# Kernel tuning notes

Measured on AMD Instinct MI355X. Metric: run time of the kernel, lower is better.

## Reference

```python
import jax, jax.numpy as jnp
import numpy as np

B, S, D, A = 16, 2048, 512, 512

def setup_inputs() -> dict:
    key = jax.random.key(0)
    ks = jax.random.split(key, 7)
    scale = 1.0 / np.sqrt(D)
    return {
        "query": jax.random.normal(ks[0], (B, S, D), dtype=jnp.float32),
        "key_": jax.random.normal(ks[1], (B, S, D), dtype=jnp.float32),
        "value": jax.random.normal(ks[2], (B, S, D), dtype=jnp.float32),
        "Wq": jax.random.normal(ks[3], (D, A), dtype=jnp.float32) * scale,
        "Wk": jax.random.normal(ks[4], (D, A), dtype=jnp.float32) * scale,
        "Wv": jax.random.normal(ks[5], (D, A), dtype=jnp.float32) * scale,
        "Ws": jax.random.normal(ks[6], (A, 1), dtype=jnp.float32) * (1.0 / np.sqrt(A)),
    }

def reference(query, key_, value, Wq, Wk, Wv, Ws):
    # Dense projections (no bias): [B,S,D] @ [D,A] -> [B,S,A]
    q = jnp.einsum("bsd,da->bsa", query, Wq)
    k = jnp.einsum("bsd,da->bsa", key_, Wk)
    v = jnp.einsum("bsd,da->bsa", value, Wv)
    # Additive (Bahdanau) scores: tanh(q+k) @ Ws -> [B,S]
    scores = jnp.einsum("bsa,a->bs", jnp.tanh(q + k), Ws[:, 0])
    attention_weights = jax.nn.softmax(scores, axis=1)[..., None]  # [B,S,1]
    context_vector = jnp.sum(attention_weights * v, axis=1)        # [B,A]
    return context_vector, attention_weights
```

## Files before the change

### kernel.cpp

```cpp
#include <hip/hip_runtime.h>
#include <hip/hip_bf16.h>
#include <stdint.h>

#define B_ 16
#define S_ 2048
#define D_ 512
#define A_ 512

typedef __attribute__((ext_vector_type(4))) float f32x4;
typedef __attribute__((ext_vector_type(8))) short bf16x8;

__device__ inline unsigned short f2bf(float f) {
  union { float f; unsigned int u; } c; c.f = f;
  unsigned int u = c.u;
  unsigned int r = (u + 0x7fffu + ((u >> 16) & 1u)) >> 16;
  return (unsigned short)r;
}

__device__ inline unsigned pk2bf(float x, float y) {
  __hip_bfloat162 p = __float22bfloat162_rn(float2{x, y});
  union { __hip_bfloat162 h; unsigned u; } c; c.h = p;
  return c.u;
}

__device__ inline float fast_tanh(float x) {
  float e = __expf(2.0f * x);
  return 1.0f - 2.0f * __builtin_amdgcn_rcpf(e + 1.0f);
}

__device__ inline void gload_lds16(const void* g, void* l) {
  __builtin_amdgcn_global_load_lds((const __attribute__((address_space(1))) void*)g,
                                   (__attribute__((address_space(3))) void*)l, 16, 0, 0);
}

__global__ __launch_bounds__(256) void k0_pack_w(const float* __restrict__ Wq,
                                                 const float* __restrict__ Wk,
                                                 unsigned short* __restrict__ WT) {
  __shared__ unsigned short tile[64][65];
  int bid = blockIdx.x;
  int dt = bid & 15, at = bid >> 4;
  int d0 = dt * 64, a0 = at * 64;
  int t = threadIdx.x;
  int col = t & 63, rbase = t >> 6;
#pragma unroll
  for (int r8 = 0; r8 < 16; ++r8) {
    int row = r8 * 4 + rbase;
    int dcat = d0 + row;
    float f = (dcat < 512) ? Wq[(size_t)dcat * 512 + a0 + col]
                           : Wk[(size_t)(dcat - 512) * 512 + a0 + col];
    tile[row][col] = f2bf(f);
  }
  __syncthreads();
#pragma unroll
  for (int r8 = 0; r8 < 16; ++r8) {
    int arow = r8 * 4 + rbase;
    WT[(size_t)(a0 + arow) * 1024 + d0 + col] = tile[col][arow];
  }
}

__global__ __launch_bounds__(512, 2) void k1_scores(
    const float* __restrict__ Q, const float* __restrict__ K,
    const unsigned short* __restrict__ WT, const float* __restrict__ Wsv,
    float* __restrict__ score) {
  __shared__ unsigned short Al[2][128 * 32];
  __shared__ unsigned short Bl[2][512 * 32];

  const int t = threadIdx.x;
  const int lane = t & 63, w = t >> 6;
  const int frow = lane & 15, fsl = lane >> 4;
  const int row0 = (int)blockIdx.x * 128;

  const int ar = t >> 2, ak = (t & 3) * 8;
  const int abyte = ar * 64 + (((t & 3) ^ ((ar >> 1) & 3)) * 16);

  float4 rA0[2], rA1[2];

  auto issueA = [&](int p, float4* r) {
    const float* src = (p < 16) ? Q : K;
    const float* ap = src + (size_t)(row0 + ar) * 512 + ((p * 32) & 511) + ak;
    r[0] = *(const float4*)(ap);
    r[1] = *(const float4*)(ap + 4);
  };
  auto writeA = [&](const float4* r, int buf) {
    uint4 d;
    d.x = pk2bf(r[0].x, r[0].y);
    d.y = pk2bf(r[0].z, r[0].w);
    d.z = pk2bf(r[1].x, r[1].y);
    d.w = pk2bf(r[1].z, r[1].w);
    *(uint4*)((char*)&Al[buf][0] + abyte) = d;
  };
  auto stageB = [&](int p, int buf) {
#pragma unroll
    for (int q = 0; q < 4; ++q) {
      int pc = (w * 4 + q) * 64 + lane;
      int row = pc >> 2;
      int sl = (pc & 3) ^ ((row >> 1) & 3);
      const char* g = (const char*)WT + (size_t)row * 2048 + p * 64 + sl * 16;
      gload_lds16(g, (char*)&Bl[buf][0] + (size_t)(w * 4 + q) * 1024);
    }
  };

  f32x4 acc[8][4];
#pragma unroll
  for (int m = 0; m < 8; ++m)
#pragma unroll
    for (int n = 0; n < 4; ++n) acc[m][n] = (f32x4){0.f, 0.f, 0.f, 0.f};

  const int ch = (fsl ^ ((frow >> 1) & 3)) * 16;

  auto doMfma = [&](int CUR) {
    bf16x8 af[8], bfr[4];
#pragma unroll
    for (int m = 0; m < 8; ++m)
      af[m] = *(const bf16x8*)((const char*)&Al[CUR][0] + (m * 16 + frow) * 64 + ch);
#pragma unroll
    for (int n = 0; n < 4; ++n)
      bfr[n] = *(const bf16x8*)((const char*)&Bl[CUR][0] + (w * 64 + n * 16 + frow) * 64 + ch);
    __builtin_amdgcn_s_setprio(1);
#pragma unroll
    for (int m = 0; m < 8; ++m)
#pragma unroll
      for (int n = 0; n < 4; ++n)
        acc[m][n] = __builtin_amdgcn_mfma_f32_16x16x32_bf16(af[m], bfr[n], acc[m][n], 0, 0, 0);
    __builtin_amdgcn_s_setprio(0);
  };

  issueA(0, rA0);
  stageB(0, 0);
  __builtin_amdgcn_sched_barrier(0);
  issueA(1, rA1);
  writeA(rA0, 0);
  asm volatile("s_waitcnt vmcnt(2) lgkmcnt(0)" ::: "memory");
  __builtin_amdgcn_s_barrier();

  auto phase = [&](int p, int CUR, float4* rCur, const float4* rNext) {
    stageB(p + 1, CUR ^ 1);
    __builtin_amdgcn_sched_barrier(0);
    issueA(p + 2, rCur);
    doMfma(CUR);
    writeA(rNext, CUR ^ 1);
    asm volatile("s_waitcnt vmcnt(2) lgkmcnt(0)" ::: "memory");
    __builtin_amdgcn_s_barrier();
  };

  for (int kt2 = 0; kt2 < 15; ++kt2) {
    phase(2 * kt2 + 0, 0, rA0, rA1);
    phase(2 * kt2 + 1, 1, rA1, rA0);
  }

  stageB(31, 1);
  doMfma(0);
  writeA(rA1, 1);
  asm volatile("s_waitcnt vmcnt(0) lgkmcnt(0)" ::: "memory");
  __builtin_amdgcn_s_barrier();
  doMfma(1);

  float wsv[4];
#pragma unroll
  for (int n = 0; n < 4; ++n) wsv[n] = Wsv[w * 64 + n * 16 + frow];
  __syncthreads();
  float* scw = (float*)&Al[0][0];
#pragma unroll
  for (int m = 0; m < 8; ++m) {
#pragma unroll
    for (int ii = 0; ii < 4; ++ii) {
      float s = 0.f;
#pragma unroll
      for (int n = 0; n < 4; ++n)
        s += fast_tanh(acc[m][n][ii]) * wsv[n];
      s += __shfl_xor(s, 1);
      s += __shfl_xor(s, 2);
      s += __shfl_xor(s, 4);
      s += __shfl_xor(s, 8);
      if (frow == 0) scw[w * 128 + m * 16 + fsl * 4 + ii] = s;
    }
  }
  __syncthreads();
  if (t < 128) {
    float s = 0.f;
#pragma unroll
    for (int ww = 0; ww < 8; ++ww) s += scw[ww * 128 + t];
    score[row0 + t] = s;
  }
}

__global__ __launch_bounds__(256) void k3_vsum(const float* __restrict__ value,
                                               const float* __restrict__ score,
                                               float* __restrict__ upart,
                                               float* __restrict__ outw) {
  int bid = blockIdx.x;
  int dh = bid & 1, sc = (bid >> 1) & 15, b = bid >> 5;
  int t = threadIdx.x;
  int lane = t & 63, wave = t >> 6;
  int dg = t & 63, sg = t >> 6;
  __shared__ float red[4], red2[4];
  __shared__ float wl[128];
  __shared__ f32x4 redv[4][64];

  float v[8];
  float mx = -1e30f;
#pragma unroll
  for (int e = 0; e < 8; ++e) {
    float p = score[(size_t)b * S_ + e * 256 + t];
    v[e] = p;
    mx = fmaxf(mx, p);
  }
  for (int off = 1; off < 64; off <<= 1) mx = fmaxf(mx, __shfl_xor(mx, off));
  if (lane == 0) red[wave] = mx;
  __syncthreads();
  mx = fmaxf(fmaxf(red[0], red[1]), fmaxf(red[2], red[3]));
  float sum = 0.f;
#pragma unroll
  for (int e = 0; e < 8; ++e) sum += expf(v[e] - mx);
  for (int off = 1; off < 64; off <<= 1) sum += __shfl_xor(sum, off);
  if (lane == 0) red2[wave] = sum;
  __syncthreads();
  sum = red2[0] + red2[1] + red2[2] + red2[3];
  float inv = 1.f / sum;

  int s0 = sc * 128;
  if (t < 128) {
    size_t o = (size_t)b * S_ + s0 + t;
    float ww = expf(score[o] - mx) * inv;
    wl[t] = ww;
    if (dh == 0) outw[o] = ww;
  }
  __syncthreads();

  const float* vp = value + ((size_t)b * S_ + s0) * 512 + dh * 256 + dg * 4;
  f32x4 a = (f32x4){0.f, 0.f, 0.f, 0.f};
  for (int s = sg; s < 128; s += 4) {
    float4 v4 = *(const float4*)(vp + (size_t)s * 512);
    float ws = wl[s];
    a[0] += ws * v4.x; a[1] += ws * v4.y; a[2] += ws * v4.z; a[3] += ws * v4.w;
  }
  redv[sg][dg] = a;
  __syncthreads();
  if (sg == 0) {
    f32x4 r = redv[0][dg] + redv[1][dg] + redv[2][dg] + redv[3][dg];
    float* dst = upart + (size_t)(sc * 16 + b) * 512 + dh * 256 + dg * 4;
    dst[0] = r[0]; dst[1] = r[1]; dst[2] = r[2]; dst[3] = r[3];
  }
}

__global__ __launch_bounds__(256) void k4_ctx(const float* __restrict__ upart,
                                              const float* __restrict__ Wv,
                                              float* __restrict__ out) {
  int b = blockIdx.x >> 2, q = blockIdx.x & 3;
  int t = threadIdx.x;
  int col = q * 128 + (t & 127), dhf = t >> 7;
  __shared__ float ul[512];
  __shared__ float part[2][128];
  for (int i = t; i < 512; i += 256) {
    float u = 0.f;
#pragma unroll
    for (int c = 0; c < 16; ++c) u += upart[(size_t)(c * 16 + b) * 512 + i];
    ul[i] = u;
  }
  __syncthreads();
  float acc = 0.f;
#pragma unroll 8
  for (int d = dhf * 256; d < dhf * 256 + 256; ++d)
    acc += ul[d] * Wv[(size_t)d * 512 + col];
  part[dhf][t & 127] = acc;
  __syncthreads();
  if (dhf == 0)
    out[(size_t)b * 512 + col] = part[0][t & 127] + part[1][t & 127];
}

extern "C" void kernel_launch(void* const* d_in, const int* in_sizes, int n_in,
                              void* d_out, int out_size, void* d_ws, size_t ws_size,
                              hipStream_t stream) {
  const float* Q  = (const float*)d_in[0];
  const float* Kk = (const float*)d_in[1];
  const float* V  = (const float*)d_in[2];
  const float* Wq = (const float*)d_in[3];
  const float* Wk = (const float*)d_in[4];
  const float* Wv = (const float*)d_in[5];
  const float* Ws = (const float*)d_in[6];
  float* out = (float*)d_out;

  char* ws = (char*)d_ws;
  unsigned short* WT = (unsigned short*)ws;
  float* score = (float*)(ws + (1 << 20));
  float* upart = (float*)(ws + (1 << 20) + (512 << 10));

  float* outw = out + B_ * A_;

  k0_pack_w<<<dim3(128), dim3(256), 0, stream>>>(Wq, Wk, WT);
  k1_scores<<<dim3(256), dim3(512), 0, stream>>>(Q, Kk, WT, Ws, score);
  k3_vsum<<<dim3(512), dim3(256), 0, stream>>>(V, score, upart, outw);
  k4_ctx<<<dim3(64), dim3(256), 0, stream>>>(upart, Wv, out);
}
```

Baseline: 85.25 us.

## Stage fp32 A tiles directly to LDS and convert to bf16 at fragment load

Replaces the register-staged A path (global load, bf16 pack, LDS store) with direct global-to-LDS loads of fp32 Q/K tiles using an XOR swizzle, converting to bf16 when reading MFMA fragments. The pipeline becomes a simple double-buffered loop waiting on all outstanding loads each iteration, and the score reduction buffer gets its own LDS array. This removes register pressure and VALU pack work from the staging path but doubles A's LDS footprint, repeats conversion in every wave, and drops the deeper prefetch overlap.

```diff
diff --git a/kernel.cpp b/kernel.cpp
--- a/kernel.cpp
+++ b/kernel.cpp
@@ -62,32 +62,26 @@
     const float* __restrict__ Q, const float* __restrict__ K,
     const unsigned short* __restrict__ WT, const float* __restrict__ Wsv,
     float* __restrict__ score) {
-  __shared__ unsigned short Al[2][128 * 32];
+  __shared__ float Af[2][128 * 32];
   __shared__ unsigned short Bl[2][512 * 32];
+  __shared__ float scw[8][128];
 
   const int t = threadIdx.x;
   const int lane = t & 63, w = t >> 6;
   const int frow = lane & 15, fsl = lane >> 4;
   const int row0 = (int)blockIdx.x * 128;
 
-  const int ar = t >> 2, ak = (t & 3) * 8;
-  const int abyte = ar * 64 + (((t & 3) ^ ((ar >> 1) & 3)) * 16);
-
-  float4 rA0[2], rA1[2];
-
-  auto issueA = [&](int p, float4* r) {
+  auto stageA = [&](int p, int buf) {
     const float* src = (p < 16) ? Q : K;
-    const float* ap = src + (size_t)(row0 + ar) * 512 + ((p * 32) & 511) + ak;
-    r[0] = *(const float4*)(ap);
-    r[1] = *(const float4*)(ap + 4);
-  };
-  auto writeA = [&](const float4* r, int buf) {
-    uint4 d;
-    d.x = pk2bf(r[0].x, r[0].y);
-    d.y = pk2bf(r[0].z, r[0].w);
-    d.z = pk2bf(r[1].x, r[1].y);
-    d.w = pk2bf(r[1].z, r[1].w);
-    *(uint4*)((char*)&Al[buf][0] + abyte) = d;
+    int kk = (p * 32) & 511;
+#pragma unroll
+    for (int q = 0; q < 2; ++q) {
+      int pc = w * 128 + q * 64 + lane;
+      int row = pc >> 3, c = pc & 7;
+      int gc = c ^ (row & 7);
+      const float* g = src + (size_t)(row0 + row) * 512 + kk + gc * 4;
+      gload_lds16(g, (char*)&Af[buf][0] + (size_t)(w * 128 + q * 64) * 16);
+    }
   };
   auto stageB = [&](int p, int buf) {
 #pragma unroll
@@ -106,16 +100,28 @@
 #pragma unroll
     for (int n = 0; n < 4; ++n) acc[m][n] = (f32x4){0.f, 0.f, 0.f, 0.f};
 
-  const int ch = (fsl ^ ((frow >> 1) & 3)) * 16;
+  const int chB = (fsl ^ ((frow >> 1) & 3)) * 16;
 
   auto doMfma = [&](int CUR) {
-    bf16x8 af[8], bfr[4];
-#pragma unroll
-    for (int m = 0; m < 8; ++m)
-      af[m] = *(const bf16x8*)((const char*)&Al[CUR][0] + (m * 16 + frow) * 64 + ch);
+    bf16x8 af[8];
+#pragma unroll
+    for (int m = 0; m < 8; ++m) {
+      int row = m * 16 + frow;
+      int c0 = (fsl * 2) ^ (row & 7);
+      const float* base = &Af[CUR][row * 32];
+      float4 lo = *(const float4*)(base + c0 * 4);
+      float4 hi = *(const float4*)(base + (c0 ^ 1) * 4);
+      union { bf16x8 v; unsigned u[4]; } cc;
+      cc.u[0] = pk2bf(lo.x, lo.y);
+      cc.u[1] = pk2bf(lo.z, lo.w);
+      cc.u[2] = pk2bf(hi.x, hi.y);
+      cc.u[3] = pk2bf(hi.z, hi.w);
+      af[m] = cc.v;
+    }
+    bf16x8 bfr[4];
 #pragma unroll
     for (int n = 0; n < 4; ++n)
-      bfr[n] = *(const bf16x8*)((const char*)&Bl[CUR][0] + (w * 64 + n * 16 + frow) * 64 + ch);
+      bfr[n] = *(const bf16x8*)((const char*)&Bl[CUR][0] + (w * 64 + n * 16 + frow) * 64 + chB);
     __builtin_amdgcn_s_setprio(1);
 #pragma unroll
     for (int m = 0; m < 8; ++m)
@@ -125,41 +131,24 @@
     __builtin_amdgcn_s_setprio(0);
   };
 
-  issueA(0, rA0);
+  stageA(0, 0);
   stageB(0, 0);
-  __builtin_amdgcn_sched_barrier(0);
-  issueA(1, rA1);
-  writeA(rA0, 0);
-  asm volatile("s_waitcnt vmcnt(2) lgkmcnt(0)" ::: "memory");
-  __builtin_amdgcn_s_barrier();
-
-  auto phase = [&](int p, int CUR, float4* rCur, const float4* rNext) {
-    stageB(p + 1, CUR ^ 1);
-    __builtin_amdgcn_sched_barrier(0);
-    issueA(p + 2, rCur);
-    doMfma(CUR);
-    writeA(rNext, CUR ^ 1);
-    asm volatile("s_waitcnt vmcnt(2) lgkmcnt(0)" ::: "memory");
-    __builtin_amdgcn_s_barrier();
-  };
-
-  for (int kt2 = 0; kt2 < 15; ++kt2) {
-    phase(2 * kt2 + 0, 0, rA0, rA1);
-    phase(2 * kt2 + 1, 1, rA1, rA0);
-  }
-
-  stageB(31, 1);
-  doMfma(0);
-  writeA(rA1, 1);
   asm volatile("s_waitcnt vmcnt(0) lgkmcnt(0)" ::: "memory");
   __builtin_amdgcn_s_barrier();
+
+  for (int kt = 0; kt < 31; ++kt) {
+    const int cur = kt & 1;
+    stageA(kt + 1, cur ^ 1);
+    stageB(kt + 1, cur ^ 1);
+    doMfma(cur);
+    asm volatile("s_waitcnt vmcnt(0) lgkmcnt(0)" ::: "memory");
+    __builtin_amdgcn_s_barrier();
+  }
   doMfma(1);
 
   float wsv[4];
 #pragma unroll
   for (int n = 0; n < 4; ++n) wsv[n] = Wsv[w * 64 + n * 16 + frow];
-  __syncthreads();
-  float* scw = (float*)&Al[0][0];
 #pragma unroll
   for (int m = 0; m < 8; ++m) {
 #pragma unroll
@@ -172,14 +161,14 @@
       s += __shfl_xor(s, 2);
       s += __shfl_xor(s, 4);
       s += __shfl_xor(s, 8);
-      if (frow == 0) scw[w * 128 + m * 16 + fsl * 4 + ii] = s;
+      if (frow == 0) scw[w][m * 16 + fsl * 4 + ii] = s;
     }
   }
   __syncthreads();
   if (t < 128) {
     float s = 0.f;
 #pragma unroll
-    for (int ww = 0; ww < 8; ++ww) s += scw[ww * 128 + t];
+    for (int ww = 0; ww < 8; ++ww) s += scw[ww][t];
     score[row0 + t] = s;
   }
 }
```

Result: slower. 104.0 us (+22.0%).

## Process two K-slices per barrier period with four-deep LDS buffering

Applied to the files above, without the earlier changes.

Restructures the k1_scores main loop so that each barrier period stages two 32-wide K slices of A and B into LDS and runs two MFMA batches, using four LDS buffers and two register sets for the A prefetch. This halves the number of block-wide barriers and lets loads for the next pair overlap with twice as much compute. The cost is doubled LDS use, which forces launch bounds down to one block per CU and so lowers occupancy. The __syncthreads before the score reduction is also removed, and that reduction writes into Al[0]; this looks safe only because the final barrier precedes the last MFMAs, which read buffers 2 and 3.

```diff
diff --git a/kernel.cpp b/kernel.cpp
--- a/kernel.cpp
+++ b/kernel.cpp
@@ -58,12 +58,12 @@
   }
 }
 
-__global__ __launch_bounds__(512, 2) void k1_scores(
+__global__ __launch_bounds__(512, 1) void k1_scores(
     const float* __restrict__ Q, const float* __restrict__ K,
     const unsigned short* __restrict__ WT, const float* __restrict__ Wsv,
     float* __restrict__ score) {
-  __shared__ unsigned short Al[2][128 * 32];
-  __shared__ unsigned short Bl[2][512 * 32];
+  __shared__ unsigned short Al[4][128 * 32];
+  __shared__ unsigned short Bl[4][512 * 32];
 
   const int t = threadIdx.x;
   const int lane = t & 63, w = t >> 6;
@@ -73,7 +73,7 @@
   const int ar = t >> 2, ak = (t & 3) * 8;
   const int abyte = ar * 64 + (((t & 3) ^ ((ar >> 1) & 3)) * 16);
 
-  float4 rA0[2], rA1[2];
+  float4 rP0[2], rP1[2], rQ0[2], rQ1[2];
 
   auto issueA = [&](int p, float4* r) {
     const float* src = (p < 16) ? Q : K;
@@ -108,14 +108,14 @@
 
   const int ch = (fsl ^ ((frow >> 1) & 3)) * 16;
 
-  auto doMfma = [&](int CUR) {
+  auto doMfma = [&](int buf) {
     bf16x8 af[8], bfr[4];
 #pragma unroll
     for (int m = 0; m < 8; ++m)
-      af[m] = *(const bf16x8*)((const char*)&Al[CUR][0] + (m * 16 + frow) * 64 + ch);
+      af[m] = *(const bf16x8*)((const char*)&Al[buf][0] + (m * 16 + frow) * 64 + ch);
 #pragma unroll
     for (int n = 0; n < 4; ++n)
-      bfr[n] = *(const bf16x8*)((const char*)&Bl[CUR][0] + (w * 64 + n * 16 + frow) * 64 + ch);
+      bfr[n] = *(const bf16x8*)((const char*)&Bl[buf][0] + (w * 64 + n * 16 + frow) * 64 + ch);
     __builtin_amdgcn_s_setprio(1);
 #pragma unroll
     for (int m = 0; m < 8; ++m)
@@ -125,40 +125,51 @@
     __builtin_amdgcn_s_setprio(0);
   };
 
-  issueA(0, rA0);
+  issueA(0, rP0);
+  issueA(1, rP1);
   stageB(0, 0);
+  stageB(1, 1);
   __builtin_amdgcn_sched_barrier(0);
-  issueA(1, rA1);
-  writeA(rA0, 0);
-  asm volatile("s_waitcnt vmcnt(2) lgkmcnt(0)" ::: "memory");
+  writeA(rP0, 0);
+  writeA(rP1, 1);
+  issueA(2, rQ0);
+  issueA(3, rQ1);
+  asm volatile("s_waitcnt vmcnt(4) lgkmcnt(0)" ::: "memory");
   __builtin_amdgcn_s_barrier();
 
-  auto phase = [&](int p, int CUR, float4* rCur, const float4* rNext) {
-    stageB(p + 1, CUR ^ 1);
+  auto period = [&](int i, const float4* Ya, const float4* Yb,
+                    float4* Xa, float4* Xb, bool last) {
+    const int cur2 = (i & 1) * 2, nxt2 = ((i + 1) & 1) * 2;
+    stageB(2 * i + 2, nxt2);
+    stageB(2 * i + 3, nxt2 + 1);
     __builtin_amdgcn_sched_barrier(0);
-    issueA(p + 2, rCur);
-    doMfma(CUR);
-    writeA(rNext, CUR ^ 1);
-    asm volatile("s_waitcnt vmcnt(2) lgkmcnt(0)" ::: "memory");
+    if (!last) {
+      issueA(2 * i + 4, Xa);
+      issueA(2 * i + 5, Xb);
+    }
+    doMfma(cur2);
+    doMfma(cur2 + 1);
+    writeA(Ya, nxt2);
+    writeA(Yb, nxt2 + 1);
+    if (!last)
+      asm volatile("s_waitcnt vmcnt(4) lgkmcnt(0)" ::: "memory");
+    else
+      asm volatile("s_waitcnt vmcnt(0) lgkmcnt(0)" ::: "memory");
     __builtin_amdgcn_s_barrier();
   };
 
-  for (int kt2 = 0; kt2 < 15; ++kt2) {
-    phase(2 * kt2 + 0, 0, rA0, rA1);
-    phase(2 * kt2 + 1, 1, rA1, rA0);
-  }
-
-  stageB(31, 1);
-  doMfma(0);
-  writeA(rA1, 1);
-  asm volatile("s_waitcnt vmcnt(0) lgkmcnt(0)" ::: "memory");
-  __builtin_amdgcn_s_barrier();
-  doMfma(1);
+  for (int ii = 0; ii < 7; ++ii) {
+    period(2 * ii,     rQ0, rQ1, rP0, rP1, false);
+    period(2 * ii + 1, rP0, rP1, rQ0, rQ1, false);
+  }
+  period(14, rQ0, rQ1, rP0, rP1, true);
+
+  doMfma(2);
+  doMfma(3);
 
   float wsv[4];
 #pragma unroll
   for (int n = 0; n < 4; ++n) wsv[n] = Wsv[w * 64 + n * 16 + frow];
-  __syncthreads();
   float* scw = (float*)&Al[0][0];
 #pragma unroll
   for (int m = 0; m < 8; ++m) {
```

New measurement: 87.89 us. 1.03x slower.

## Retile score GEMM to 256x256 blocks with column-split partial scores

Applied to the files above, without the earlier changes.

The fused projection-and-score kernel moves from 128-row by 512-column tiles to square 256x256 tiles. Each block now covers half of the attention dimension and writes a partial score, and the softmax kernel adds the two partials. Block indices are remapped so the two column halves of a row strip land on the same XCD, so the second read of the fp32 query and key rows should hit L2. The square tile lowers LDS staging per MFMA, at the cost of reading the activation rows twice and holding more A-prefetch registers per thread.

```diff
diff --git a/kernel.cpp b/kernel.cpp
--- a/kernel.cpp
+++ b/kernel.cpp
@@ -6,6 +6,7 @@
 #define S_ 2048
 #define D_ 512
 #define A_ 512
+#define M_TOT (B_ * S_)
 
 typedef __attribute__((ext_vector_type(4))) float f32x4;
 typedef __attribute__((ext_vector_type(8))) short bf16x8;
@@ -61,42 +62,51 @@
 __global__ __launch_bounds__(512, 2) void k1_scores(
     const float* __restrict__ Q, const float* __restrict__ K,
     const unsigned short* __restrict__ WT, const float* __restrict__ Wsv,
-    float* __restrict__ score) {
-  __shared__ unsigned short Al[2][128 * 32];
-  __shared__ unsigned short Bl[2][512 * 32];
+    float* __restrict__ partial) {
+  __shared__ unsigned short Al[2][256 * 32];
+  __shared__ unsigned short Bl[2][256 * 32];
 
   const int t = threadIdx.x;
   const int lane = t & 63, w = t >> 6;
   const int frow = lane & 15, fsl = lane >> 4;
-  const int row0 = (int)blockIdx.x * 128;
-
-  const int ar = t >> 2, ak = (t & 3) * 8;
-  const int abyte = ar * 64 + (((t & 3) ^ ((ar >> 1) & 3)) * 16);
-
-  float4 rA0[2], rA1[2];
+  const int wr = w >> 2, wc = w & 3;
+
+  const int bid = (int)blockIdx.x;
+  const int wg = (bid & 7) * 32 + (bid >> 3);
+  const int strip = wg >> 1, cb = wg & 1;
+  const int row0 = strip * 256, col0 = cb * 256;
+
+  const int ar = t >> 1, ac0 = (t & 1) * 2;
+  const int ab0 = ar * 64 + (((ac0 + 0) ^ ((ar >> 1) & 3)) * 16);
+  const int ab1 = ar * 64 + (((ac0 + 1) ^ ((ar >> 1) & 3)) * 16);
+
+  float4 rP[4], rQr[4];
 
   auto issueA = [&](int p, float4* r) {
     const float* src = (p < 16) ? Q : K;
-    const float* ap = src + (size_t)(row0 + ar) * 512 + ((p * 32) & 511) + ak;
-    r[0] = *(const float4*)(ap);
+    const float* ap = src + (size_t)(row0 + ar) * 512 + ((p * 32) & 511) + ac0 * 8;
+    r[0] = *(const float4*)(ap + 0);
     r[1] = *(const float4*)(ap + 4);
+    r[2] = *(const float4*)(ap + 8);
+    r[3] = *(const float4*)(ap + 12);
   };
   auto writeA = [&](const float4* r, int buf) {
-    uint4 d;
-    d.x = pk2bf(r[0].x, r[0].y);
-    d.y = pk2bf(r[0].z, r[0].w);
-    d.z = pk2bf(r[1].x, r[1].y);
-    d.w = pk2bf(r[1].z, r[1].w);
-    *(uint4*)((char*)&Al[buf][0] + abyte) = d;
+    uint4 d0, d1;
+    d0.x = pk2bf(r[0].x, r[0].y); d0.y = pk2bf(r[0].z, r[0].w);
+    d0.z = pk2bf(r[1].x, r[1].y); d0.w = pk2bf(r[1].z, r[1].w);
+    d1.x = pk2bf(r[2].x, r[2].y); d1.y = pk2bf(r[2].z, r[2].w);
+    d1.z = pk2bf(r[3].x, r[3].y); d1.w = pk2bf(r[3].z, r[3].w);
+    *(uint4*)((char*)&Al[buf][0] + ab0) = d0;
+    *(uint4*)((char*)&Al[buf][0] + ab1) = d1;
   };
   auto stageB = [&](int p, int buf) {
 #pragma unroll
-    for (int q = 0; q < 4; ++q) {
-      int pc = (w * 4 + q) * 64 + lane;
+    for (int q = 0; q < 2; ++q) {
+      int pc = (w * 2 + q) * 64 + lane;
       int row = pc >> 2;
       int sl = (pc & 3) ^ ((row >> 1) & 3);
-      const char* g = (const char*)WT + (size_t)row * 2048 + p * 64 + sl * 16;
-      gload_lds16(g, (char*)&Bl[buf][0] + (size_t)(w * 4 + q) * 1024);
+      const char* g = (const char*)WT + (size_t)(col0 + row) * 2048 + p * 64 + sl * 16;
+      gload_lds16(g, (char*)&Bl[buf][0] + (size_t)(w * 2 + q) * 1024);
     }
   };
 
@@ -111,11 +121,17 @@
   auto doMfma = [&](int CUR) {
     bf16x8 af[8], bfr[4];
 #pragma unroll
-    for (int m = 0; m < 8; ++m)
-      af[m] = *(const bf16x8*)((const char*)&Al[CUR][0] + (m * 16 + frow) * 64 + ch);
-#pragma unroll
-    for (int n = 0; n < 4; ++n)
-      bfr[n] = *(const bf16x8*)((const char*)&Bl[CUR][0] + (w * 64 + n * 16 + frow) * 64 + ch);
+    for (int m = 0; m < 8; ++m) {
+      int r = wr * 128 + m * 16 + frow;
+      af[m] = *(const bf16x8*)((const char*)&Al[CUR][0] + r * 64
+                               + ((fsl ^ ((r >> 1) & 3)) * 16));
+    }
+#pragma unroll
+    for (int n = 0; n < 4; ++n) {
+      int r = wc * 64 + n * 16 + frow;
+      bfr[n] = *(const bf16x8*)((const char*)&Bl[CUR][0] + r * 64
+                                + ((fsl ^ ((r >> 1) & 3)) * 16));
+    }
     __builtin_amdgcn_s_setprio(1);
 #pragma unroll
     for (int m = 0; m < 8; ++m)
@@ -125,12 +141,12 @@
     __builtin_amdgcn_s_setprio(0);
   };
 
-  issueA(0, rA0);
+  issueA(0, rP);
   stageB(0, 0);
   __builtin_amdgcn_sched_barrier(0);
-  issueA(1, rA1);
-  writeA(rA0, 0);
-  asm volatile("s_waitcnt vmcnt(2) lgkmcnt(0)" ::: "memory");
+  issueA(1, rQr);
+  writeA(rP, 0);
+  asm volatile("s_waitcnt vmcnt(4) lgkmcnt(0)" ::: "memory");
   __builtin_amdgcn_s_barrier();
 
   auto phase = [&](int p, int CUR, float4* rCur, const float4* rNext) {
@@ -139,25 +155,25 @@
     issueA(p + 2, rCur);
     doMfma(CUR);
     writeA(rNext, CUR ^ 1);
-    asm volatile("s_waitcnt vmcnt(2) lgkmcnt(0)" ::: "memory");
+    asm volatile("s_waitcnt vmcnt(4) lgkmcnt(0)" ::: "memory");
     __builtin_amdgcn_s_barrier();
   };
 
   for (int kt2 = 0; kt2 < 15; ++kt2) {
-    phase(2 * kt2 + 0, 0, rA0, rA1);
-    phase(2 * kt2 + 1, 1, rA1, rA0);
+    phase(2 * kt2 + 0, 0, rP, rQr);
+    phase(2 * kt2 + 1, 1, rQr, rP);
   }
 
   stageB(31, 1);
   doMfma(0);
-  writeA(rA1, 1);
+  writeA(rQr, 1);
   asm volatile("s_waitcnt vmcnt(0) lgkmcnt(0)" ::: "memory");
   __builtin_amdgcn_s_barrier();
   doMfma(1);
 
   float wsv[4];
 #pragma unroll
-  for (int n = 0; n < 4; ++n) wsv[n] = Wsv[w * 64 + n * 16 + frow];
+  for (int n = 0; n < 4; ++n) wsv[n] = Wsv[col0 + wc * 64 + n * 16 + frow];
   __syncthreads();
   float* scw = (float*)&Al[0][0];
 #pragma unroll
@@ -172,20 +188,19 @@
       s += __shfl_xor(s, 2);
       s += __shfl_xor(s, 4);
       s += __shfl_xor(s, 8);
-      if (frow == 0) scw[w * 128 + m * 16 + fsl * 4 + ii] = s;
+      if (frow == 0)
+        scw[wc * 256 + wr * 128 + m * 16 + fsl * 4 + ii] = s;
     }
   }
   __syncthreads();
-  if (t < 128) {
-    float s = 0.f;
-#pragma unroll
-    for (int ww = 0; ww < 8; ++ww) s += scw[ww * 128 + t];
-    score[row0 + t] = s;
+  if (t < 256) {
+    float s = scw[t] + scw[256 + t] + scw[512 + t] + scw[768 + t];
+    partial[(size_t)cb * M_TOT + row0 + t] = s;
   }
 }
 
 __global__ __launch_bounds__(256) void k3_vsum(const float* __restrict__ value,
-                                               const float* __restrict__ score,
+                                               const float* __restrict__ partial,
                                                float* __restrict__ upart,
                                                float* __restrict__ outw) {
   int bid = blockIdx.x;
@@ -201,7 +216,8 @@
   float mx = -1e30f;
 #pragma unroll
   for (int e = 0; e < 8; ++e) {
-    float p = score[(size_t)b * S_ + e * 256 + t];
+    size_t o = (size_t)b * S_ + e * 256 + t;
+    float p = partial[o] + partial[M_TOT + o];
     v[e] = p;
     mx = fmaxf(mx, p);
   }
@@ -221,7 +237,7 @@
   int s0 = sc * 128;
   if (t < 128) {
     size_t o = (size_t)b * S_ + s0 + t;
-    float ww = expf(score[o] - mx) * inv;
+    float ww = expf(partial[o] + partial[M_TOT + o] - mx) * inv;
     wl[t] = ww;
     if (dh == 0) outw[o] = ww;
   }
@@ -282,13 +298,13 @@
 
   char* ws = (char*)d_ws;
   unsigned short* WT = (unsigned short*)ws;
-  float* score = (float*)(ws + (1 << 20));
-  float* upart = (float*)(ws + (1 << 20) + (512 << 10));
+  float* partial = (float*)(ws + (1 << 20));
+  float* upart   = (float*)(ws + (1 << 20) + (512 << 10));
 
   float* outw = out + B_ * A_;
 
   k0_pack_w<<<dim3(128), dim3(256), 0, stream>>>(Wq, Wk, WT);
-  k1_scores<<<dim3(256), dim3(512), 0, stream>>>(Q, Kk, WT, Ws, score);
-  k3_vsum<<<dim3(512), dim3(256), 0, stream>>>(V, score, upart, outw);
+  k1_scores<<<dim3(256), dim3(512), 0, stream>>>(Q, Kk, WT, Ws, partial);
+  k3_vsum<<<dim3(512), dim3(256), 0, stream>>>(V, partial, upart, outw);
   k4_ctx<<<dim3(64), dim3(256), 0, stream>>>(upart, Wv, out);
 }
```

Measured after the change: 88.64 us. 1.04x slower.
